# Kernel optimization log

Measured on AMD Instinct MI355X. Metric: run time of the kernel, lower is better.

Reference implementation:

```python
import jax, jax.numpy as jnp
import numpy as np

NS = 0.4      # neighborhood_size
GS = 8        # grid_size
RNN = 128     # rnn_size
EMB = 64      # embedding_size
NMIX = 20     # nmixtures
N = 1024      # num pedestrians


def setup_inputs() -> dict:
    key = jax.random.key(0)
    ks = jax.random.split(key, 14)
    s = 0.05
    return {
        "xoff": jax.random.normal(ks[0], (N, 2)) * s,
        "xabs": jax.random.uniform(ks[1], (N, 2)),
        "h0": jax.random.normal(ks[2], (1, N, RNN)) * 0.1,
        "c0": jax.random.normal(ks[3], (1, N, RNN)) * 0.1,
        "W_emb": jax.random.normal(ks[4], (EMB, 2)) * s,
        "b_emb": jax.random.normal(ks[5], (EMB,)) * s,
        "W_soc": jax.random.normal(ks[6], (EMB, GS * GS * RNN)) * s,
        "b_soc": jax.random.normal(ks[7], (EMB,)) * s,
        "W_ih": jax.random.normal(ks[8], (4 * RNN, 2 * EMB)) * s,
        "W_hh": jax.random.normal(ks[9], (4 * RNN, RNN)) * s,
        "b_ih": jax.random.normal(ks[10], (4 * RNN,)) * s,
        "b_hh": jax.random.normal(ks[11], (4 * RNN,)) * s,
        "W_out": jax.random.normal(ks[12], (6 * NMIX, RNN)) * s,
        "b_out": jax.random.normal(ks[13], (6 * NMIX,)) * s,
    }


def grid_mask(xabs, dtype):
    # Vectorized getGridMask: [N, N, GS*GS] one-hot neighbor binning.
    x, y = xabs[:, 0], xabs[:, 1]
    dx = x[None, :] - (x[:, None] - NS / 2)  # other_x - width_low, [N, N]
    dy = y[None, :] - (y[:, None] - NS / 2)
    cx = jnp.floor(dx / NS * GS).astype(jnp.int32)
    cy = jnp.floor(dy / NS * GS).astype(jnp.int32)
    n = x.shape[0]
    valid = ((dx >= 0) & (dx < NS) & (dy >= 0) & (dy < NS)
             & (cx >= 0) & (cx < GS) & (cy >= 0) & (cy < GS)
             & ~jnp.eye(n, dtype=bool))
    cell = jnp.clip(cx + cy * GS, 0, GS * GS - 1)
    return jax.nn.one_hot(cell, GS * GS, dtype=dtype) * valid[..., None].astype(dtype)


def reference(xoff, xabs, h0, c0, W_emb, b_emb, W_soc, b_soc,
              W_ih, W_hh, b_ih, b_hh, W_out, b_out):
    n = xabs.shape[0]
    # predict_distance=True -> embed offsets
    emb = jax.nn.relu(xoff @ W_emb.T + b_emb)                 # [N, 64]
    grid = grid_mask(xabs, emb.dtype)                          # [N, N, 64]
    h = h0[0]                                                  # [N, 128]
    # getSocialTensor: scatter neighbor hidden states into grid bins
    social = jnp.einsum('nmg,mh->ngh', grid, h).reshape(n, GS * GS * RNN)
    pool = jax.nn.relu(social @ W_soc.T + b_soc)               # [N, 64]
    xin = jnp.concatenate([emb, pool], axis=-1)                # [N, 128]
    # single-step LSTM, torch gate order i, f, g, o
    gates = xin @ W_ih.T + h @ W_hh.T + b_ih + b_hh            # [N, 512]
    i, f, g, o = jnp.split(gates, 4, axis=-1)
    c = jax.nn.sigmoid(f) * c0[0] + jax.nn.sigmoid(i) * jnp.tanh(g)
    hn = jax.nn.sigmoid(o) * jnp.tanh(c)
    out = hn @ W_out.T + b_out                                 # [N, 120]
    mu1, mu2, ls1, ls2, rho, pi_logits = jnp.split(out, 6, axis=1)
    return (mu1, mu2, ls1, ls2, rho, pi_logits)
```

## Files before the change

kernel.cpp:

```cpp
#include <hip/hip_runtime.h>
#include <hip/hip_bf16.h>

#define NN_ 1024

#define U_WGF  0
#define U_SHI  131072
#define U_ACTH 655360
#define U_P    917504
#define F_WOUT 2555904
#define F_HN   2572288

typedef __attribute__((ext_vector_type(8))) short short8;
typedef __attribute__((ext_vector_type(4))) float floatx4;

__device__ __forceinline__ float b2f_(unsigned short u) {
    return __uint_as_float(((unsigned)u) << 16);
}
__device__ __forceinline__ unsigned short f2bu(float f) {
    __hip_bfloat16 b = __float2bfloat16(f);
    return *(unsigned short*)&b;
}
__device__ __forceinline__ float ldin(const void* p, int i, int isbf) {
    return isbf ? b2f_(((const unsigned short*)p)[i]) : ((const float*)p)[i];
}
__device__ __forceinline__ int detect_bf16(const void* Wih, int tid) {
    unsigned wv = ((const unsigned*)Wih)[tid];
    unsigned e8 = (wv >> 7) & 0xFFu;
    return (__syncthreads_count((e8 >= 96u && e8 <= 134u) ? 1 : 0) > 128) ? 1 : 0;
}

__global__ __launch_bounds__(256) void prep_kernel(
        const void* __restrict__ xoff, const void* __restrict__ h0,
        const void* __restrict__ Wsoc, const void* __restrict__ Wemb,
        const void* __restrict__ bemb, const void* __restrict__ Wih,
        const void* __restrict__ Whh,  const void* __restrict__ Wout,
        float* __restrict__ ws) {
    const int tid = threadIdx.x;
    const int isbf = detect_bf16(Wih, tid);
    unsigned short* u = (unsigned short*)ws;
    const int t0 = (blockIdx.x * 256 + tid) * 8;
    unsigned short hv[8];
    if (t0 < 131072) {
        int jl = (t0 >> 3) & 15, q = (t0 >> 7) & 3, kb = (t0 >> 9) & 7, jt = t0 >> 12;
        int j = (jt & 3) * 128 + (jt >> 2) * 16 + jl;
        int k0 = kb * 32 + q * 8;
#pragma unroll
        for (int r = 0; r < 8; r++) {
            int k = k0 + r;
            float v = (k < 128) ? ldin(Wih, j * 128 + k, isbf)
                                : ldin(Whh, j * 128 + (k - 128), isbf);
            hv[r] = f2bu(v);
        }
        *(short8*)(u + U_WGF + t0) = *(short8*)hv;
    } else if (t0 < 147456) {
        int t2 = t0 - 131072; int r = t2 >> 7, j0 = t2 & 127;
#pragma unroll
        for (int i = 0; i < 8; i++) {
            int j = j0 + i;
            ws[F_WOUT + t2 + i] = (j < 120) ? ldin(Wout, j * 128 + r, isbf) : 0.0f;
        }
    } else if (t0 < 671744) {
        int t2 = t0 - 147456;
        int e = (t2 >> 3) & 63, q = (t2 >> 9) & 3, j = (t2 >> 11) & 3, g = t2 >> 13;
        int src = e * 8192 + g * 128 + j * 32 + q * 8;
#pragma unroll
        for (int r = 0; r < 8; r++) hv[r] = f2bu(ldin(Wsoc, src + r, isbf));
        *(short8*)(u + U_SHI + t2) = *(short8*)hv;
    } else if (t0 < 802816) {
        int t2 = t0 - 671744; int n = t2 >> 7, k = t2 & 127;
#pragma unroll
        for (int i = 0; i < 8; i++) hv[i] = f2bu(ldin(h0, t2 + i, isbf));
        *(short8*)(u + U_ACTH + n * 256 + 128 + k) = *(short8*)hv;
    } else {
        int t2 = t0 - 802816; int n = t2 >> 6, e0 = t2 & 63;
        float x0 = ldin(xoff, 2 * n, isbf), x1 = ldin(xoff, 2 * n + 1, isbf);
#pragma unroll
        for (int i = 0; i < 8; i++) {
            int e = e0 + i;
            float v = fmaf(x0, ldin(Wemb, 2 * e, isbf),
                      fmaf(x1, ldin(Wemb, 2 * e + 1, isbf), ldin(bemb, e, isbf)));
            hv[i] = f2bu(fmaxf(v, 0.0f));
        }
        *(short8*)(u + U_ACTH + n * 256 + e0) = *(short8*)hv;
    }
}

__global__ __launch_bounds__(256) void pgemm_kernel(float* __restrict__ ws) {
    const unsigned short* u = (const unsigned short*)ws;
    const short* Ah  = (const short*)(u + U_ACTH);
    const short* Shi = (const short*)(u + U_SHI);
    unsigned short* P16 = (unsigned short*)ws + U_P;
    const int tid = threadIdx.x, lane = tid & 63, wv = tid >> 6;
    const int B_ = blockIdx.y * 64 + blockIdx.x;
    const int mtile = B_ & 63, rest = B_ >> 6;
    const int cg = rest >> 1, thalf = rest & 1;
    const int m = lane & 15, q = lane >> 4;
    const int g = cg * 4 + wv;
    const int abase = (mtile * 16 + m) * 256 + 128 + q * 8;
    short8 ah[4];
#pragma unroll
    for (int j = 0; j < 4; j++) ah[j] = *(const short8*)(Ah + abase + 32 * j);
    const int rowl = mtile * 16 + q * 4;
#pragma unroll
    for (int tt = 0; tt < 2; tt++) {
        const int t = thalf * 2 + tt;
        const int e = t * 16 + m;
        floatx4 c = {0.0f, 0.0f, 0.0f, 0.0f};
#pragma unroll
        for (int j = 0; j < 4; j++) {
            short8 bh = *(const short8*)(Shi + ((g * 4 + j) * 4 + q) * 512 + e * 8);
            c = __builtin_amdgcn_mfma_f32_16x16x32_bf16(ah[j], bh, c, 0, 0, 0);
        }
        const int n0 = cg * 256 + wv * 64 + t * 16;
#pragma unroll
        for (int r = 0; r < 4; r++)
            P16[(rowl + r) * 4096 + n0 + m] = f2bu(c[r]);
    }
}

__global__ __launch_bounds__(256) void pool_kernel(const void* __restrict__ xabs,
                                                   const void* __restrict__ b_soc,
                                                   const void* __restrict__ Wih_det,
                                                   float* __restrict__ ws) {
    __shared__ float xabs_s[2048];
    __shared__ int   off[NN_];
    __shared__ int   cnt_s;
    __shared__ float4 red4[16][16];
    const int tid = threadIdx.x;
    const int isbf = detect_bf16(Wih_det, tid);
    const int n = blockIdx.x;
    unsigned short* u = (unsigned short*)ws;

    for (int i = tid; i < 2048; i += 256) xabs_s[i] = ldin(xabs, i, isbf);
    if (tid == 0) cnt_s = 0;
    __syncthreads();
    {
        float xs = xabs_s[2 * n]     - 0.2f;
        float ys = xabs_s[2 * n + 1] - 0.2f;
        for (int i = tid; i < NN_; i += 256) {
            float dx = xabs_s[2 * i]     - xs;
            float dy = xabs_s[2 * i + 1] - ys;
            int cx = (int)floorf(dx / 0.4f * 8.0f);
            int cy = (int)floorf(dy / 0.4f * 8.0f);
            bool valid = (dx >= 0.0f) && (dx < 0.4f) && (dy >= 0.0f) && (dy < 0.4f)
                      && (cx >= 0) && (cx < 8) && (cy >= 0) && (cy < 8) && (i != n);
            if (valid) {
                int idx = atomicAdd(&cnt_s, 1);
                off[idx] = i * 4096 + ((cy * 8 + cx) << 6);
            }
        }
    }
    __syncthreads();
    {
        const unsigned short* P16 = (const unsigned short*)ws + U_P;
        const int strm = tid >> 4, e4 = tid & 15;
        const int cc = cnt_s;
        float ax = 0.0f, ay = 0.0f, az = 0.0f, aw = 0.0f;
        for (int j = strm; j < cc; j += 16) {
            int o = off[j];
            ushort4 uu = *(const ushort4*)(P16 + o + 4 * e4);
            ax += b2f_(uu.x); ay += b2f_(uu.y); az += b2f_(uu.z); aw += b2f_(uu.w);
        }
        red4[strm][e4] = make_float4(ax, ay, az, aw);
    }
    __syncthreads();
    if (tid < 16) {
        float s[4] = {0.0f, 0.0f, 0.0f, 0.0f};
#pragma unroll
        for (int s16 = 0; s16 < 16; s16++) {
            float4 r = red4[s16][tid];
            s[0] += r.x; s[1] += r.y; s[2] += r.z; s[3] += r.w;
        }
        int e = 4 * tid;
#pragma unroll
        for (int i = 0; i < 4; i++) {
            float v = fmaxf(s[i] + ldin(b_soc, e + i, isbf), 0.0f);
            u[U_ACTH + n * 256 + 64 + e + i] = f2bu(v);
        }
    }
}

__global__ __launch_bounds__(256) void gates_kernel(const void* __restrict__ c0,
                                                    const void* __restrict__ b_ih,
                                                    const void* __restrict__ b_hh,
                                                    const void* __restrict__ Wih_det,
                                                    float* __restrict__ ws) {
    __shared__ float gl[16][68];
    const int tid = threadIdx.x;
    const int isbf = detect_bf16(Wih_det, tid);
    const unsigned short* u = (const unsigned short*)ws;
    const short* Ah = (const short*)(u + U_ACTH);
    const short* Wg = (const short*)(u + U_WGF);
    const int lane = tid & 63, wv = tid >> 6, m = lane & 15, q = lane >> 4;
    const int m0 = blockIdx.x * 16, y = blockIdx.y;
    const int jt = y * 4 + wv;
    floatx4 acc = {0.0f, 0.0f, 0.0f, 0.0f};
#pragma unroll
    for (int kb = 0; kb < 8; kb++) {
        short8 ah = *(const short8*)(Ah + (m0 + m) * 256 + kb * 32 + q * 8);
        short8 b  = *(const short8*)(Wg + (jt * 8 + kb) * 512 + q * 128 + m * 8);
        acc = __builtin_amdgcn_mfma_f32_16x16x32_bf16(ah, b, acc, 0, 0, 0);
    }
    const int jorig = wv * 128 + y * 16 + m;
    const float bias = ldin(b_ih, jorig, isbf) + ldin(b_hh, jorig, isbf);
#pragma unroll
    for (int r = 0; r < 4; r++)
        gl[q * 4 + r][wv * 16 + m] = acc[r] + bias;
    __syncthreads();
    {
        const int a = tid >> 4, rl = tid & 15;
        const int n = m0 + a, rg = y * 16 + rl;
        float iv = gl[a][rl],      fv = gl[a][16 + rl];
        float gv = gl[a][32 + rl], ov = gl[a][48 + rl];
        float si = 1.0f / (1.0f + expf(-iv));
        float sf = 1.0f / (1.0f + expf(-fv));
        float so = 1.0f / (1.0f + expf(-ov));
        float cc = sf * ldin(c0, n * 128 + rg, isbf) + si * tanhf(gv);
        ws[F_HN + n * 128 + rg] = so * tanhf(cc);
    }
}

__global__ __launch_bounds__(256) void pwout_kernel(const void* __restrict__ b_out,
                                                    const void* __restrict__ Wih_det,
                                                    const float* __restrict__ ws,
                                                    float* __restrict__ out) {
    __shared__ __align__(16) float hnl[2][128];
    const int tid = threadIdx.x;
    const int isbf = detect_bf16(Wih_det, tid);
    const int n0 = blockIdx.x * 2;
    const int half = tid >> 7, t2 = tid & 127;
    const int n = n0 + half;
    hnl[half][t2] = ws[F_HN + n * 128 + t2];
    __syncthreads();
    if (t2 < 120) {
        int j = t2;
        float acc = ldin(b_out, j, isbf);
        for (int r = 0; r < 128; r += 4) {
            float4 hq = *(const float4*)&hnl[half][r];
            acc = fmaf(hq.x, ws[F_WOUT + (r + 0) * 128 + j], acc);
            acc = fmaf(hq.y, ws[F_WOUT + (r + 1) * 128 + j], acc);
            acc = fmaf(hq.z, ws[F_WOUT + (r + 2) * 128 + j], acc);
            acc = fmaf(hq.w, ws[F_WOUT + (r + 3) * 128 + j], acc);
        }
        int ch = j / 20, wc = j - ch * 20;
        out[ch * 20480 + n * 20 + wc] = acc;
    }
}

extern "C" void kernel_launch(void* const* d_in, const int* in_sizes, int n_in,
                              void* d_out, int out_size, void* d_ws, size_t ws_size,
                              hipStream_t stream) {
    const void* xoff  = d_in[0];
    const void* xabs  = d_in[1];
    const void* h0    = d_in[2];
    const void* c0    = d_in[3];
    const void* W_emb = d_in[4];
    const void* b_emb = d_in[5];
    const void* W_soc = d_in[6];
    const void* b_soc = d_in[7];
    const void* W_ih  = d_in[8];
    const void* W_hh  = d_in[9];
    const void* b_ih  = d_in[10];
    const void* b_hh  = d_in[11];
    const void* W_out = d_in[12];
    const void* b_out = d_in[13];
    float* ws = (float*)d_ws;
    float* out = (float*)d_out;

    prep_kernel<<<424, 256, 0, stream>>>(xoff, h0, W_soc, W_emb, b_emb,
                                         W_ih, W_hh, W_out, ws);
    pgemm_kernel<<<dim3(64, 32), 256, 0, stream>>>(ws);
    pool_kernel<<<1024, 256, 0, stream>>>(xabs, b_soc, W_ih, ws);
    gates_kernel<<<dim3(64, 8), 256, 0, stream>>>(c0, b_ih, b_hh, W_ih, ws);
    pwout_kernel<<<512, 256, 0, stream>>>(b_out, W_ih, ws, out);
}
```

Baseline: 117.9 us.

## Fuse five kernels into two: merged prep/GEMM/binning and pool+LSTM+output

Replaces the five-kernel pipeline with two launches. The first kernel computes the h0·W_soc projection straight from the raw inputs, with no separate bf16 staging pass, and in the same launch builds per-pedestrian neighbor offset lists and repacks the LSTM and output weights. The second kernel pools the neighbor contributions, builds the LSTM input in a swizzled LDS tile, runs the gate MFMA, the activations and the output projection for 4 pedestrians per block. This removes launch overhead and intermediate global round trips. The cost is that the gate MFMA pads 16 rows for only 4 real ones, and the per-block work in the second kernel is more serial.

```diff
diff --git a/kernel.cpp b/kernel.cpp
--- a/kernel.cpp
+++ b/kernel.cpp
@@ -3,15 +3,16 @@
 
 #define NN_ 1024
 
-#define U_WGF  0
-#define U_SHI  131072
-#define U_ACTH 655360
-#define U_P    917504
-#define F_WOUT 2555904
-#define F_HN   2572288
+#define U_WGF   0
+#define F_WOUT  65536
+#define U_P     163840
+#define I_OFF   2179072
+#define I_CNT   3227648
 
 typedef __attribute__((ext_vector_type(8))) short short8;
 typedef __attribute__((ext_vector_type(4))) float floatx4;
+
+#define AT(r,c) ((((r)<<9) + ((c)<<1)) ^ (((r)&7)<<4))
 
 __device__ __forceinline__ float b2f_(unsigned short u) {
     return __uint_as_float(((unsigned)u) << 16);
@@ -28,222 +29,233 @@
     unsigned e8 = (wv >> 7) & 0xFFu;
     return (__syncthreads_count((e8 >= 96u && e8 <= 134u) ? 1 : 0) > 128) ? 1 : 0;
 }
-
-__global__ __launch_bounds__(256) void prep_kernel(
-        const void* __restrict__ xoff, const void* __restrict__ h0,
-        const void* __restrict__ Wsoc, const void* __restrict__ Wemb,
-        const void* __restrict__ bemb, const void* __restrict__ Wih,
+__device__ __forceinline__ short8 ld8_bf(const void* p, int idx, int isbf) {
+    if (isbf) return *(const short8*)((const unsigned short*)p + idx);
+    const float4* f = (const float4*)((const float*)p + idx);
+    float4 a = f[0], b = f[1];
+    short8 r;
+    r[0] = (short)f2bu(a.x); r[1] = (short)f2bu(a.y);
+    r[2] = (short)f2bu(a.z); r[3] = (short)f2bu(a.w);
+    r[4] = (short)f2bu(b.x); r[5] = (short)f2bu(b.y);
+    r[6] = (short)f2bu(b.z); r[7] = (short)f2bu(b.w);
+    return r;
+}
+
+__global__ __launch_bounds__(256) void fused1_kernel(
+        const void* __restrict__ xabs, const void* __restrict__ h0,
+        const void* __restrict__ Wsoc, const void* __restrict__ Wih,
         const void* __restrict__ Whh,  const void* __restrict__ Wout,
         float* __restrict__ ws) {
     const int tid = threadIdx.x;
+    const int bid = blockIdx.x;
     const int isbf = detect_bf16(Wih, tid);
     unsigned short* u = (unsigned short*)ws;
-    const int t0 = (blockIdx.x * 256 + tid) * 8;
-    unsigned short hv[8];
-    if (t0 < 131072) {
-        int jl = (t0 >> 3) & 15, q = (t0 >> 7) & 3, kb = (t0 >> 9) & 7, jt = t0 >> 12;
-        int j = (jt & 3) * 128 + (jt >> 2) * 16 + jl;
-        int k0 = kb * 32 + q * 8;
-#pragma unroll
-        for (int r = 0; r < 8; r++) {
-            int k = k0 + r;
-            float v = (k < 128) ? ldin(Wih, j * 128 + k, isbf)
-                                : ldin(Whh, j * 128 + (k - 128), isbf);
-            hv[r] = f2bu(v);
-        }
-        *(short8*)(u + U_WGF + t0) = *(short8*)hv;
-    } else if (t0 < 147456) {
-        int t2 = t0 - 131072; int r = t2 >> 7, j0 = t2 & 127;
-#pragma unroll
-        for (int i = 0; i < 8; i++) {
-            int j = j0 + i;
-            ws[F_WOUT + t2 + i] = (j < 120) ? ldin(Wout, j * 128 + r, isbf) : 0.0f;
-        }
-    } else if (t0 < 671744) {
-        int t2 = t0 - 147456;
-        int e = (t2 >> 3) & 63, q = (t2 >> 9) & 3, j = (t2 >> 11) & 3, g = t2 >> 13;
-        int src = e * 8192 + g * 128 + j * 32 + q * 8;
-#pragma unroll
-        for (int r = 0; r < 8; r++) hv[r] = f2bu(ldin(Wsoc, src + r, isbf));
-        *(short8*)(u + U_SHI + t2) = *(short8*)hv;
-    } else if (t0 < 802816) {
-        int t2 = t0 - 671744; int n = t2 >> 7, k = t2 & 127;
-#pragma unroll
-        for (int i = 0; i < 8; i++) hv[i] = f2bu(ldin(h0, t2 + i, isbf));
-        *(short8*)(u + U_ACTH + n * 256 + 128 + k) = *(short8*)hv;
-    } else {
-        int t2 = t0 - 802816; int n = t2 >> 6, e0 = t2 & 63;
-        float x0 = ldin(xoff, 2 * n, isbf), x1 = ldin(xoff, 2 * n + 1, isbf);
-#pragma unroll
-        for (int i = 0; i < 8; i++) {
-            int e = e0 + i;
-            float v = fmaf(x0, ldin(Wemb, 2 * e, isbf),
-                      fmaf(x1, ldin(Wemb, 2 * e + 1, isbf), ldin(bemb, e, isbf)));
-            hv[i] = f2bu(fmaxf(v, 0.0f));
-        }
-        *(short8*)(u + U_ACTH + n * 256 + e0) = *(short8*)hv;
-    }
-}
-
-__global__ __launch_bounds__(256) void pgemm_kernel(float* __restrict__ ws) {
-    const unsigned short* u = (const unsigned short*)ws;
-    const short* Ah  = (const short*)(u + U_ACTH);
-    const short* Shi = (const short*)(u + U_SHI);
-    unsigned short* P16 = (unsigned short*)ws + U_P;
-    const int tid = threadIdx.x, lane = tid & 63, wv = tid >> 6;
-    const int B_ = blockIdx.y * 64 + blockIdx.x;
-    const int mtile = B_ & 63, rest = B_ >> 6;
-    const int cg = rest >> 1, thalf = rest & 1;
-    const int m = lane & 15, q = lane >> 4;
-    const int g = cg * 4 + wv;
-    const int abase = (mtile * 16 + m) * 256 + 128 + q * 8;
-    short8 ah[4];
-#pragma unroll
-    for (int j = 0; j < 4; j++) ah[j] = *(const short8*)(Ah + abase + 32 * j);
-    const int rowl = mtile * 16 + q * 4;
-#pragma unroll
-    for (int tt = 0; tt < 2; tt++) {
-        const int t = thalf * 2 + tt;
-        const int e = t * 16 + m;
-        floatx4 c = {0.0f, 0.0f, 0.0f, 0.0f};
-#pragma unroll
-        for (int j = 0; j < 4; j++) {
-            short8 bh = *(const short8*)(Shi + ((g * 4 + j) * 4 + q) * 512 + e * 8);
-            c = __builtin_amdgcn_mfma_f32_16x16x32_bf16(ah[j], bh, c, 0, 0, 0);
-        }
-        const int n0 = cg * 256 + wv * 64 + t * 16;
-#pragma unroll
-        for (int r = 0; r < 4; r++)
-            P16[(rowl + r) * 4096 + n0 + m] = f2bu(c[r]);
-    }
-}
-
-__global__ __launch_bounds__(256) void pool_kernel(const void* __restrict__ xabs,
-                                                   const void* __restrict__ b_soc,
-                                                   const void* __restrict__ Wih_det,
-                                                   float* __restrict__ ws) {
-    __shared__ float xabs_s[2048];
-    __shared__ int   off[NN_];
-    __shared__ int   cnt_s;
-    __shared__ float4 red4[16][16];
-    const int tid = threadIdx.x;
-    const int isbf = detect_bf16(Wih_det, tid);
-    const int n = blockIdx.x;
-    unsigned short* u = (unsigned short*)ws;
-
-    for (int i = tid; i < 2048; i += 256) xabs_s[i] = ldin(xabs, i, isbf);
-    if (tid == 0) cnt_s = 0;
-    __syncthreads();
-    {
-        float xs = xabs_s[2 * n]     - 0.2f;
-        float ys = xabs_s[2 * n + 1] - 0.2f;
-        for (int i = tid; i < NN_; i += 256) {
-            float dx = xabs_s[2 * i]     - xs;
-            float dy = xabs_s[2 * i + 1] - ys;
+
+    if (bid < 512) {
+        unsigned short* P16 = u + U_P;
+        const int mg = bid >> 4, ng = bid & 15;
+        const int lane = tid & 63, wv = tid >> 6;
+        const int m = lane & 15, q = lane >> 4;
+        short8 ah[2][4];
+#pragma unroll
+        for (int mt = 0; mt < 2; ++mt) {
+            const int row = mg * 32 + mt * 16 + m;
+#pragma unroll
+            for (int kb = 0; kb < 4; ++kb)
+                ah[mt][kb] = ld8_bf(h0, row * 128 + kb * 32 + q * 8, isbf);
+        }
+#pragma unroll
+        for (int c = 0; c < 4; ++c) {
+            const int ct = wv * 4 + c;
+            const int col = ng * 256 + ct * 16 + m;
+            const int g = col >> 6, e = col & 63;
+            short8 bf[4];
+#pragma unroll
+            for (int kb = 0; kb < 4; ++kb)
+                bf[kb] = ld8_bf(Wsoc, e * 8192 + g * 128 + kb * 32 + q * 8, isbf);
+            floatx4 c0_ = {0.f, 0.f, 0.f, 0.f}, c1_ = {0.f, 0.f, 0.f, 0.f};
+#pragma unroll
+            for (int kb = 0; kb < 4; ++kb) {
+                c0_ = __builtin_amdgcn_mfma_f32_16x16x32_bf16(ah[0][kb], bf[kb], c0_, 0, 0, 0);
+                c1_ = __builtin_amdgcn_mfma_f32_16x16x32_bf16(ah[1][kb], bf[kb], c1_, 0, 0, 0);
+            }
+#pragma unroll
+            for (int r = 0; r < 4; ++r) {
+                P16[(mg * 32 + q * 4 + r) * 4096 + col]      = f2bu(c0_[r]);
+                P16[(mg * 32 + 16 + q * 4 + r) * 4096 + col] = f2bu(c1_[r]);
+            }
+        }
+    } else if (bid < 768) {
+        __shared__ float xs_[2048];
+        __shared__ int cnt_s[4];
+        for (int i = tid; i < 2048; i += 256) xs_[i] = ldin(xabs, i, isbf);
+        if (tid < 4) cnt_s[tid] = 0;
+        __syncthreads();
+        const int a = tid >> 6, t = tid & 63;
+        const int n = (bid - 512) * 4 + a;
+        unsigned* OFF = (unsigned*)ws + I_OFF + n * 1024;
+        const float xsn = xs_[2 * n]     - 0.2f;
+        const float ysn = xs_[2 * n + 1] - 0.2f;
+        for (int i = t; i < NN_; i += 64) {
+            float dx = xs_[2 * i]     - xsn;
+            float dy = xs_[2 * i + 1] - ysn;
             int cx = (int)floorf(dx / 0.4f * 8.0f);
             int cy = (int)floorf(dy / 0.4f * 8.0f);
             bool valid = (dx >= 0.0f) && (dx < 0.4f) && (dy >= 0.0f) && (dy < 0.4f)
                       && (cx >= 0) && (cx < 8) && (cy >= 0) && (cy < 8) && (i != n);
             if (valid) {
-                int idx = atomicAdd(&cnt_s, 1);
-                off[idx] = i * 4096 + ((cy * 8 + cx) << 6);
-            }
-        }
-    }
-    __syncthreads();
-    {
-        const unsigned short* P16 = (const unsigned short*)ws + U_P;
-        const int strm = tid >> 4, e4 = tid & 15;
-        const int cc = cnt_s;
-        float ax = 0.0f, ay = 0.0f, az = 0.0f, aw = 0.0f;
-        for (int j = strm; j < cc; j += 16) {
-            int o = off[j];
-            ushort4 uu = *(const ushort4*)(P16 + o + 4 * e4);
-            ax += b2f_(uu.x); ay += b2f_(uu.y); az += b2f_(uu.z); aw += b2f_(uu.w);
-        }
-        red4[strm][e4] = make_float4(ax, ay, az, aw);
-    }
-    __syncthreads();
-    if (tid < 16) {
-        float s[4] = {0.0f, 0.0f, 0.0f, 0.0f};
-#pragma unroll
-        for (int s16 = 0; s16 < 16; s16++) {
-            float4 r = red4[s16][tid];
-            s[0] += r.x; s[1] += r.y; s[2] += r.z; s[3] += r.w;
-        }
-        int e = 4 * tid;
-#pragma unroll
-        for (int i = 0; i < 4; i++) {
-            float v = fmaxf(s[i] + ldin(b_soc, e + i, isbf), 0.0f);
-            u[U_ACTH + n * 256 + 64 + e + i] = f2bu(v);
-        }
-    }
-}
-
-__global__ __launch_bounds__(256) void gates_kernel(const void* __restrict__ c0,
-                                                    const void* __restrict__ b_ih,
-                                                    const void* __restrict__ b_hh,
-                                                    const void* __restrict__ Wih_det,
-                                                    float* __restrict__ ws) {
-    __shared__ float gl[16][68];
+                int pos = atomicAdd(&cnt_s[a], 1);
+                OFF[pos] = (unsigned)(i * 4096 + ((cy * 8 + cx) << 6));
+            }
+        }
+        __syncthreads();
+        if (tid < 4) ((unsigned*)ws)[I_CNT + (bid - 512) * 4 + tid] = (unsigned)cnt_s[tid];
+    } else if (bid < 832) {
+        const int t0 = (bid - 768) * 2048 + tid * 8;
+        const int jl = (t0 >> 3) & 15, qq = (t0 >> 7) & 3, kb = (t0 >> 9) & 7, jt = t0 >> 12;
+        const int j = (jt & 3) * 128 + (jt >> 2) * 16 + jl;
+        const int k0 = kb * 32 + qq * 8;
+        unsigned short hv[8];
+#pragma unroll
+        for (int r = 0; r < 8; ++r) {
+            int k = k0 + r;
+            float v = (k < 128) ? ldin(Wih, j * 128 + k, isbf)
+                                : ldin(Whh, j * 128 + (k - 128), isbf);
+            hv[r] = f2bu(v);
+        }
+        *(short8*)(u + U_WGF + t0) = *(short8*)hv;
+    } else {
+        const int t2 = (bid - 832) * 2048 + tid * 8;
+        const int r = t2 >> 7, j0 = t2 & 127;
+#pragma unroll
+        for (int i = 0; i < 8; ++i) {
+            int j = j0 + i;
+            ws[F_WOUT + t2 + i] = (j < 120) ? ldin(Wout, j * 128 + r, isbf) : 0.0f;
+        }
+    }
+}
+
+__global__ __launch_bounds__(256) void fused2_kernel(
+        const void* __restrict__ xoff, const void* __restrict__ h0,
+        const void* __restrict__ c0,   const void* __restrict__ Wemb,
+        const void* __restrict__ bemb, const void* __restrict__ bsoc,
+        const void* __restrict__ bih,  const void* __restrict__ bhh,
+        const void* __restrict__ bout, const void* __restrict__ Wih_det,
+        const float* __restrict__ ws,  float* __restrict__ out) {
+    __shared__ __align__(16) unsigned short At[4096];
+    __shared__ float red[4][8][64];
+    __shared__ float gl[4][512];
+    __shared__ __align__(16) float hnl[4][128];
     const int tid = threadIdx.x;
     const int isbf = detect_bf16(Wih_det, tid);
-    const unsigned short* u = (const unsigned short*)ws;
-    const short* Ah = (const short*)(u + U_ACTH);
-    const short* Wg = (const short*)(u + U_WGF);
-    const int lane = tid & 63, wv = tid >> 6, m = lane & 15, q = lane >> 4;
-    const int m0 = blockIdx.x * 16, y = blockIdx.y;
-    const int jt = y * 4 + wv;
-    floatx4 acc = {0.0f, 0.0f, 0.0f, 0.0f};
-#pragma unroll
-    for (int kb = 0; kb < 8; kb++) {
-        short8 ah = *(const short8*)(Ah + (m0 + m) * 256 + kb * 32 + q * 8);
-        short8 b  = *(const short8*)(Wg + (jt * 8 + kb) * 512 + q * 128 + m * 8);
-        acc = __builtin_amdgcn_mfma_f32_16x16x32_bf16(ah, b, acc, 0, 0, 0);
-    }
-    const int jorig = wv * 128 + y * 16 + m;
-    const float bias = ldin(b_ih, jorig, isbf) + ldin(b_hh, jorig, isbf);
-#pragma unroll
-    for (int r = 0; r < 4; r++)
-        gl[q * 4 + r][wv * 16 + m] = acc[r] + bias;
-    __syncthreads();
-    {
-        const int a = tid >> 4, rl = tid & 15;
-        const int n = m0 + a, rg = y * 16 + rl;
-        float iv = gl[a][rl],      fv = gl[a][16 + rl];
-        float gv = gl[a][32 + rl], ov = gl[a][48 + rl];
+    const int n0 = blockIdx.x * 4;
+    char* atb = (char*)At;
+    const unsigned short* P16 = (const unsigned short*)ws + U_P;
+
+    {
+        const int a = tid >> 6, s = (tid >> 3) & 7, l = tid & 7;
+        const unsigned cnt = ((const unsigned*)ws)[I_CNT + n0 + a];
+        const unsigned* lst = (const unsigned*)ws + I_OFF + (n0 + a) * 1024;
+        float acc[8] = {0.f, 0.f, 0.f, 0.f, 0.f, 0.f, 0.f, 0.f};
+        unsigned j = s;
+        while (j + 24 < cnt) {
+            unsigned o0 = lst[j], o1 = lst[j + 8], o2 = lst[j + 16], o3 = lst[j + 24];
+            short8 v0 = *(const short8*)(P16 + o0 + l * 8);
+            short8 v1 = *(const short8*)(P16 + o1 + l * 8);
+            short8 v2 = *(const short8*)(P16 + o2 + l * 8);
+            short8 v3 = *(const short8*)(P16 + o3 + l * 8);
+#pragma unroll
+            for (int i = 0; i < 8; ++i)
+                acc[i] += b2f_((unsigned short)v0[i]) + b2f_((unsigned short)v1[i])
+                        + b2f_((unsigned short)v2[i]) + b2f_((unsigned short)v3[i]);
+            j += 32;
+        }
+        while (j < cnt) {
+            unsigned o0 = lst[j];
+            short8 v0 = *(const short8*)(P16 + o0 + l * 8);
+#pragma unroll
+            for (int i = 0; i < 8; ++i) acc[i] += b2f_((unsigned short)v0[i]);
+            j += 8;
+        }
+#pragma unroll
+        for (int i = 0; i < 8; ++i) red[a][s][l * 8 + i] = acc[i];
+    }
+    __syncthreads();
+    {
+        const int a = tid >> 6, e = tid & 63;
+        float p = 0.f;
+#pragma unroll
+        for (int s = 0; s < 8; ++s) p += red[a][s][e];
+        p += ldin(bsoc, e, isbf);
+        *(unsigned short*)(atb + AT(a, 64 + e)) = f2bu(fmaxf(p, 0.0f));
+        float x0 = ldin(xoff, 2 * (n0 + a), isbf), x1 = ldin(xoff, 2 * (n0 + a) + 1, isbf);
+        float v = fmaf(x0, ldin(Wemb, 2 * e, isbf),
+                  fmaf(x1, ldin(Wemb, 2 * e + 1, isbf), ldin(bemb, e, isbf)));
+        *(unsigned short*)(atb + AT(a, e)) = f2bu(fmaxf(v, 0.0f));
+    }
+    for (int z = tid; z < 512; z += 256) {
+        int a = z >> 7, k = z & 127;
+        *(unsigned short*)(atb + AT(a, 128 + k)) = f2bu(ldin(h0, (n0 + a) * 128 + k, isbf));
+    }
+    for (int z = tid; z < 3072; z += 256) {
+        int row = 4 + (z >> 8), col = z & 255;
+        *(unsigned short*)(atb + AT(row, col)) = 0;
+    }
+    __syncthreads();
+    {
+        const int lane = tid & 63, wv = tid >> 6, m = lane & 15, q = lane >> 4;
+        short8 af[8];
+#pragma unroll
+        for (int kb = 0; kb < 8; ++kb)
+            af[kb] = *(const short8*)(atb + AT(m, kb * 32 + q * 8));
+        const short* Wg = (const short*)((const unsigned short*)ws + U_WGF);
+#pragma unroll
+        for (int y2 = 0; y2 < 8; ++y2) {
+            floatx4 c = {0.f, 0.f, 0.f, 0.f};
+#pragma unroll
+            for (int kb = 0; kb < 8; ++kb) {
+                short8 b = *(const short8*)(Wg + ((y2 * 4 + wv) * 8 + kb) * 512 + q * 128 + m * 8);
+                c = __builtin_amdgcn_mfma_f32_16x16x32_bf16(af[kb], b, c, 0, 0, 0);
+            }
+            if (q == 0) {
+                const int jor = wv * 128 + y2 * 16 + m;
+                const float bias = ldin(bih, jor, isbf) + ldin(bhh, jor, isbf);
+#pragma unroll
+                for (int r = 0; r < 4; ++r)
+                    gl[r][wv * 128 + y2 * 16 + m] = c[r] + bias;
+            }
+        }
+    }
+    __syncthreads();
+    for (int z = tid; z < 512; z += 256) {
+        const int a = z >> 7, r = z & 127, n = n0 + a;
+        float iv = gl[a][r],       fv = gl[a][128 + r];
+        float gv = gl[a][256 + r], ov = gl[a][384 + r];
         float si = 1.0f / (1.0f + expf(-iv));
         float sf = 1.0f / (1.0f + expf(-fv));
         float so = 1.0f / (1.0f + expf(-ov));
-        float cc = sf * ldin(c0, n * 128 + rg, isbf) + si * tanhf(gv);
-        ws[F_HN + n * 128 + rg] = so * tanhf(cc);
-    }
-}
-
-__global__ __launch_bounds__(256) void pwout_kernel(const void* __restrict__ b_out,
-                                                    const void* __restrict__ Wih_det,
-                                                    const float* __restrict__ ws,
-                                                    float* __restrict__ out) {
-    __shared__ __align__(16) float hnl[2][128];
-    const int tid = threadIdx.x;
-    const int isbf = detect_bf16(Wih_det, tid);
-    const int n0 = blockIdx.x * 2;
-    const int half = tid >> 7, t2 = tid & 127;
-    const int n = n0 + half;
-    hnl[half][t2] = ws[F_HN + n * 128 + t2];
-    __syncthreads();
-    if (t2 < 120) {
-        int j = t2;
-        float acc = ldin(b_out, j, isbf);
-        for (int r = 0; r < 128; r += 4) {
-            float4 hq = *(const float4*)&hnl[half][r];
-            acc = fmaf(hq.x, ws[F_WOUT + (r + 0) * 128 + j], acc);
-            acc = fmaf(hq.y, ws[F_WOUT + (r + 1) * 128 + j], acc);
-            acc = fmaf(hq.z, ws[F_WOUT + (r + 2) * 128 + j], acc);
-            acc = fmaf(hq.w, ws[F_WOUT + (r + 3) * 128 + j], acc);
-        }
-        int ch = j / 20, wc = j - ch * 20;
-        out[ch * 20480 + n * 20 + wc] = acc;
+        float cc = sf * ldin(c0, n * 128 + r, isbf) + si * tanhf(gv);
+        hnl[a][r] = so * tanhf(cc);
+    }
+    __syncthreads();
+    {
+        const int jj = tid & 127, a2 = tid >> 7;
+        if (jj < 120) {
+            const int ch = jj / 20, wc = jj - ch * 20;
+#pragma unroll
+            for (int ai = 0; ai < 2; ++ai) {
+                const int a = a2 + ai * 2, n = n0 + a;
+                float acc2 = ldin(bout, jj, isbf);
+                for (int r = 0; r < 128; r += 4) {
+                    float4 hq = *(const float4*)&hnl[a][r];
+                    acc2 = fmaf(hq.x, ws[F_WOUT + (r + 0) * 128 + jj], acc2);
+                    acc2 = fmaf(hq.y, ws[F_WOUT + (r + 1) * 128 + jj], acc2);
+                    acc2 = fmaf(hq.z, ws[F_WOUT + (r + 2) * 128 + jj], acc2);
+                    acc2 = fmaf(hq.w, ws[F_WOUT + (r + 3) * 128 + jj], acc2);
+                }
+                out[ch * 20480 + n * 20 + wc] = acc2;
+            }
+        }
     }
 }
 
@@ -267,10 +279,7 @@
     float* ws = (float*)d_ws;
     float* out = (float*)d_out;
 
-    prep_kernel<<<424, 256, 0, stream>>>(xoff, h0, W_soc, W_emb, b_emb,
-                                         W_ih, W_hh, W_out, ws);
-    pgemm_kernel<<<dim3(64, 32), 256, 0, stream>>>(ws);
-    pool_kernel<<<1024, 256, 0, stream>>>(xabs, b_soc, W_ih, ws);
-    gates_kernel<<<dim3(64, 8), 256, 0, stream>>>(c0, b_ih, b_hh, W_ih, ws);
-    pwout_kernel<<<512, 256, 0, stream>>>(b_out, W_ih, ws, out);
-}
+    fused1_kernel<<<840, 256, 0, stream>>>(xabs, h0, W_soc, W_ih, W_hh, W_out, ws);
+    fused2_kernel<<<256, 256, 0, stream>>>(xoff, h0, c0, W_emb, b_emb, b_soc,
+                                           b_ih, b_hh, b_out, W_ih, ws, out);
+}
```

New measurement: 120.8 us. +2.5%, slower.
